# Kernel optimization log

Measured on AMD Instinct MI355X. Metric: run time of the kernel, lower is better.

The kernel has to match this reference:

```python
import jax, jax.numpy as jnp
import numpy as np

B, S, V, I, H = 32, 512, 8000, 256, 512
LN_EPS = 1e-5


def setup_inputs() -> dict:
    key = jax.random.key(0)
    ks = jax.random.split(key, 8)
    norm = lambda k, shp, sc: jax.random.normal(k, shp, dtype=jnp.float32) * sc
    return {
        "x_idx": jax.random.randint(ks[0], (B, S), 0, V),
        "emb": norm(ks[1], (V, I), 1.0),                    # nn.Embedding weight
        "W_in": norm(ks[2], (H, I), 1.0 / np.sqrt(I)),       # input_proj
        "b_in": jnp.zeros((H,), jnp.float32),
        "W_rec": norm(ks[3], (H, H), 1.0 / np.sqrt(H)),      # recurrent_proj
        "b_rec": jnp.zeros((H,), jnp.float32),
        "W_tr": norm(ks[4], (H, H), 1.0 / np.sqrt(H)),       # trunk linear
        "b_tr": jnp.zeros((H,), jnp.float32),
        "gamma": jnp.ones((H,), jnp.float32),                # shared LayerNorm
        "beta": jnp.zeros((H,), jnp.float32),
        "W_out": norm(ks[5], (V, H), 1.0 / np.sqrt(H)),      # output_proj
        "b_out": jnp.zeros((V,), jnp.float32),
    }


def reference(x_idx, emb, W_in, b_in, W_rec, b_rec, W_tr, b_tr, gamma, beta, W_out, b_out):
    bsz = x_idx.shape[0]

    def layer_norm(x):
        m = jnp.mean(x, axis=-1, keepdims=True)
        v = jnp.mean((x - m) ** 2, axis=-1, keepdims=True)
        return (x - m) * jax.lax.rsqrt(v + LN_EPS) * gamma + beta

    xs = emb[x_idx]                     # [B,S,I] gather all embeddings up front
    xs_t = jnp.swapaxes(xs, 0, 1)       # [S,B,I] for scan over time

    def step(h, x_t):
        h_t = jnp.tanh(x_t @ W_in.T + b_in + h @ W_rec.T + b_rec)   # [B,H]
        h_new = layer_norm(jnp.tanh(h_t @ W_tr.T + b_tr))           # trunk (layer_count=1)
        return h_new, h_new

    h0 = jnp.zeros((bsz, W_in.shape[0]), xs.dtype)
    _, hs = jax.lax.scan(step, h0, xs_t)                            # hs: [S,B,H]

    # output projection is out of the recurrence -> batch it after the scan
    y_s = jnp.einsum('sbh,vh->bsv', hs, W_out) + b_out              # [B,S,V]
    return y_s
```

## Files before the change

### kernel.cpp

```cpp
#include <hip/hip_runtime.h>
#include <hip/hip_bf16.h>

#define B_ 32
#define S_ 512
#define V_ 8000
#define I_ 256
#define H_ 512
#define LN_EPS 1e-5f
#define NSL 16
#define NBP 8
#define NBLK 128
#define PHALF (NBP * NSL * 4 * 512)

#define OFF_WR   0
#define OFF_WT   16512
#define OFF_HB   33024
#define OFF_HTS  35088
#define OFF_RED  35220
#define OFF_RED2 37268
#define LDSF     37284

static __device__ __forceinline__ unsigned short f2bf(float x) {
    __hip_bfloat16 h = __float2bfloat16(x);
    return *reinterpret_cast<unsigned short*>(&h);
}

__global__ void k_transpose(const float* __restrict__ in, float* __restrict__ out,
                            int R, int C) {
    __shared__ float tile[32][33];
    int c0 = blockIdx.x * 32, r0 = blockIdx.y * 32;
    int tx = threadIdx.x, ty = threadIdx.y;
#pragma unroll
    for (int i = 0; i < 32; i += 8)
        tile[ty + i][tx] = in[(size_t)(r0 + ty + i) * C + (c0 + tx)];
    __syncthreads();
#pragma unroll
    for (int i = 0; i < 32; i += 8)
        out[(size_t)(c0 + ty + i) * R + (r0 + tx)] = tile[tx][ty + i];
}

__global__ __launch_bounds__(256) void k_cvt_bf16(const float* __restrict__ in,
                                                  unsigned short* __restrict__ out, int n4) {
    for (int i = blockIdx.x * 256 + threadIdx.x; i < n4; i += gridDim.x * 256) {
        float4 v = ((const float4*)in)[i];
        ushort4 o;
        o.x = f2bf(v.x); o.y = f2bf(v.y); o.z = f2bf(v.z); o.w = f2bf(v.w);
        ((ushort4*)out)[i] = o;
    }
}

__global__ __launch_bounds__(512) void k_embed_proj(
        const int* __restrict__ x_idx, const float* __restrict__ emb,
        const float* __restrict__ WinT, const float* __restrict__ b_in,
        float* __restrict__ Xp) {
    __shared__ float e[8][I_];
    const int m0 = blockIdx.x * 8;
    const int t = threadIdx.x;
    {
        int r = t >> 6, i4 = (t & 63) * 4;
        int m = m0 + r;
        int s = m >> 5, b = m & 31;
        int idx = x_idx[b * S_ + s];
        *(float4*)&e[r][i4] = *(const float4*)&emb[(size_t)idx * I_ + i4];
    }
    __syncthreads();
    const int j = t;
    float acc[8];
    const float bj = b_in[j];
#pragma unroll
    for (int r = 0; r < 8; ++r) acc[r] = bj;
    for (int i = 0; i < I_; ++i) {
        float w = WinT[(size_t)i * H_ + j];
#pragma unroll
        for (int r = 0; r < 8; ++r) acc[r] += e[r][i] * w;
    }
#pragma unroll
    for (int r = 0; r < 8; ++r)
        Xp[(size_t)(m0 + r) * H_ + j] = acc[r];
}

__global__ __launch_bounds__(512) void k_scan_1b(
        const float* __restrict__ Xp,
        const float* __restrict__ W_rec, const float* __restrict__ b_rec,
        const float* __restrict__ W_tr,  const float* __restrict__ b_tr,
        const float* __restrict__ gamma, const float* __restrict__ beta,
        float* __restrict__ pP, unsigned int* __restrict__ flags,
        unsigned short* __restrict__ hsB) {
    extern __shared__ float sm[];
    float*  WrS  = sm + OFF_WR;
    float*  WtS  = sm + OFF_WT;
    float*  hb   = sm + OFF_HB;
    float*  hts  = sm + OFF_HTS;
    float*  red  = sm + OFF_RED;
    float2* red2 = (float2*)(sm + OFF_RED2);

    const int bid = blockIdx.x;
    const int bp = bid >> 4, g = bid & 15;
    const int t = threadIdx.x;
    const int j = t & 31, kc = t >> 5;
    const int rB = t >> 7, jB = (t & 127) << 2;
    const int wid = t >> 6;

    for (int idx = t; idx < 32 * 512; idx += 512) {
        int jj = idx >> 9, k = idx & 511;
        WrS[jj * 516 + k] = W_rec[(size_t)(g * 32 + jj) * H_ + k];
    }
    for (int idx = t; idx < 512 * 32; idx += 512) {
        int jj = idx >> 5, kl = idx & 31;
        WtS[kl * 516 + jj] = W_tr[(size_t)jj * H_ + g * 32 + kl];
    }
    const float brj = b_rec[g * 32 + j];
    const float4 bt4 = *(const float4*)&b_tr[jB];
    const float4 gm4 = *(const float4*)&gamma[jB];
    const float4 be4 = *(const float4*)&beta[jB];
    __syncthreads();

    for (int s = 0; s < S_; ++s) {
        float xv = 0.f;
        if (t < 128) xv = Xp[((size_t)s * B_ + bp * 4 + (t >> 5)) * H_ + g * 32 + (t & 31)];

        {
            float a0 = 0, a1 = 0, a2 = 0, a3 = 0;
            if (s > 0) {
                const int kbase = kc * 32;
#pragma unroll
                for (int i = 0; i < 8; ++i) {
                    const int k4 = kbase + i * 4;
                    const float4 w4 = *(const float4*)&WrS[j * 516 + k4];
                    const float4 h0 = *(const float4*)&hb[0 * 516 + k4];
                    const float4 h1 = *(const float4*)&hb[1 * 516 + k4];
                    const float4 h2 = *(const float4*)&hb[2 * 516 + k4];
                    const float4 h3 = *(const float4*)&hb[3 * 516 + k4];
                    a0 += h0.x * w4.x + h0.y * w4.y + h0.z * w4.z + h0.w * w4.w;
                    a1 += h1.x * w4.x + h1.y * w4.y + h1.z * w4.z + h1.w * w4.w;
                    a2 += h2.x * w4.x + h2.y * w4.y + h2.z * w4.z + h2.w * w4.w;
                    a3 += h3.x * w4.x + h3.y * w4.y + h3.z * w4.z + h3.w * w4.w;
                }
            }
            red[kc * 128 + 0 * 32 + j] = a0;
            red[kc * 128 + 1 * 32 + j] = a1;
            red[kc * 128 + 2 * 32 + j] = a2;
            red[kc * 128 + 3 * 32 + j] = a3;
        }
        __syncthreads();
        if (t < 128) {
            const int r2 = t >> 5, j2 = t & 31;
            float sum = 0.f;
#pragma unroll
            for (int c = 0; c < 16; ++c) sum += red[c * 128 + r2 * 32 + j2];
            hts[r2 * 33 + j2] = tanhf(sum + xv + brj);
        }
        __syncthreads();

        {
            float4 pa = {0.f, 0.f, 0.f, 0.f};
            const float* hrow = hts + rB * 33;
#pragma unroll 8
            for (int kl = 0; kl < 32; ++kl) {
                const float hv = hrow[kl];
                const float4 w4 = *(const float4*)&WtS[kl * 516 + jB];
                pa.x += hv * w4.x; pa.y += hv * w4.y;
                pa.z += hv * w4.z; pa.w += hv * w4.w;
            }
            const size_t pb = (size_t)(s & 1) * PHALF
                            + (size_t)(bp * 16 + g) * 2048 + rB * 512 + jB;
            union { float2 f; unsigned long long u; } q0, q1;
            q0.f = make_float2(pa.x, pa.y);
            q1.f = make_float2(pa.z, pa.w);
            __hip_atomic_store((unsigned long long*)&pP[pb], q0.u,
                               __ATOMIC_RELAXED, __HIP_MEMORY_SCOPE_AGENT);
            __hip_atomic_store((unsigned long long*)&pP[pb + 2], q1.u,
                               __ATOMIC_RELAXED, __HIP_MEMORY_SCOPE_AGENT);
        }
        __syncthreads();

        if (t == 0)
            __hip_atomic_store(&flags[(bp * 16 + g) * 32], (unsigned)(s + 1),
                               __ATOMIC_RELEASE, __HIP_MEMORY_SCOPE_AGENT);
        if (t < NSL)
            while (__hip_atomic_load(&flags[(bp * 16 + t) * 32],
                       __ATOMIC_RELAXED, __HIP_MEMORY_SCOPE_AGENT) < (unsigned)(s + 1))
                __builtin_amdgcn_s_sleep(1);
        __syncthreads();
        __builtin_amdgcn_sched_barrier(0);

        float u0, u1, u2, u3;
        {
            float a0 = 0, a1 = 0, a2 = 0, a3 = 0;
            const unsigned long long* gp =
                (const unsigned long long*)(pP + (size_t)(s & 1) * PHALF);
            const int off = rB * 512 + jB;
#pragma unroll
            for (int gg = 0; gg < 16; ++gg) {
                const size_t base = ((size_t)(bp * 16 + gg) * 2048 + off) >> 1;
                unsigned long long v0 = __hip_atomic_load(&gp[base],
                                           __ATOMIC_RELAXED, __HIP_MEMORY_SCOPE_AGENT);
                unsigned long long v1 = __hip_atomic_load(&gp[base + 1],
                                           __ATOMIC_RELAXED, __HIP_MEMORY_SCOPE_AGENT);
                union { unsigned long long u; float2 f; } w0, w1;
                w0.u = v0; w1.u = v1;
                a0 += w0.f.x; a1 += w0.f.y; a2 += w1.f.x; a3 += w1.f.y;
            }
            u0 = tanhf(a0 + bt4.x); u1 = tanhf(a1 + bt4.y);
            u2 = tanhf(a2 + bt4.z); u3 = tanhf(a3 + bt4.w);
            float s1 = (u0 + u1) + (u2 + u3);
            float s2 = (u0 * u0 + u1 * u1) + (u2 * u2 + u3 * u3);
#pragma unroll
            for (int o = 1; o < 64; o <<= 1) {
                s1 += __shfl_xor(s1, o);
                s2 += __shfl_xor(s2, o);
            }
            if ((t & 63) == 0) red2[wid] = make_float2(s1, s2);
        }
        __syncthreads();

        {
            const float2 A = red2[rB * 2], Bv = red2[rB * 2 + 1];
            const float mean = (A.x + Bv.x) * (1.0f / H_);
            const float var  = (A.y + Bv.y) * (1.0f / H_) - mean * mean;
            const float rs = rsqrtf(var + LN_EPS);
            float4 hn;
            hn.x = (u0 - mean) * rs * gm4.x + be4.x;
            hn.y = (u1 - mean) * rs * gm4.y + be4.y;
            hn.z = (u2 - mean) * rs * gm4.z + be4.z;
            hn.w = (u3 - mean) * rs * gm4.w + be4.w;
            *(float4*)&hb[rB * 516 + jB] = hn;
            if ((jB >> 5) == g) {
                ushort4 o;
                o.x = f2bf(hn.x); o.y = f2bf(hn.y);
                o.z = f2bf(hn.z); o.w = f2bf(hn.w);
                *(ushort4*)&hsB[((size_t)s * B_ + bp * 4 + rB) * H_ + jB] = o;
            }
        }
        __syncthreads();
    }
}

typedef __attribute__((ext_vector_type(8))) short short8;
typedef __attribute__((ext_vector_type(4))) float f32x4;

__global__ __launch_bounds__(256) void k_out_mfma(
        const unsigned short* __restrict__ hsB, const unsigned short* __restrict__ WoB,
        const float* __restrict__ b_out, float* __restrict__ y) {
    __shared__ unsigned short As[128 * 40];
    __shared__ unsigned short Bs[128 * 40];

    const int v0 = blockIdx.x * 128;
    const int m0 = blockIdx.y * 128;
    const int t = threadIdx.x;
    const int l = t & 63, wv = t >> 6;
    const int wm = wv >> 1, wn = wv & 1;

    f32x4 acc[4][4];
#pragma unroll
    for (int i = 0; i < 4; ++i)
#pragma unroll
        for (int jq = 0; jq < 4; ++jq)
            acc[i][jq] = (f32x4){0.f, 0.f, 0.f, 0.f};

    float bias[4];
#pragma unroll
    for (int ni = 0; ni < 4; ++ni) {
        int v = v0 + wn * 64 + ni * 16 + (l & 15);
        bias[ni] = (v < V_) ? b_out[v] : 0.f;
    }

    for (int k0 = 0; k0 < H_; k0 += 32) {
        __syncthreads();
        for (int c = t; c < 512; c += 256) {
            int row = c >> 2, seg = c & 3;
            *(uint4*)&As[row * 40 + seg * 8] =
                *(const uint4*)&hsB[(size_t)(m0 + row) * H_ + k0 + seg * 8];
            int vr = v0 + row; if (vr > V_ - 1) vr = V_ - 1;
            *(uint4*)&Bs[row * 40 + seg * 8] =
                *(const uint4*)&WoB[(size_t)vr * H_ + k0 + seg * 8];
        }
        __syncthreads();

        short8 af[4], bf[4];
#pragma unroll
        for (int i = 0; i < 4; ++i) {
            af[i] = *(short8*)&As[(wm * 64 + i * 16 + (l & 15)) * 40 + (l >> 4) * 8];
            bf[i] = *(short8*)&Bs[(wn * 64 + i * 16 + (l & 15)) * 40 + (l >> 4) * 8];
        }
#pragma unroll
        for (int mi = 0; mi < 4; ++mi)
#pragma unroll
            for (int ni = 0; ni < 4; ++ni)
                acc[mi][ni] = __builtin_amdgcn_mfma_f32_16x16x32_bf16(
                    af[mi], bf[ni], acc[mi][ni], 0, 0, 0);
    }

#pragma unroll
    for (int mi = 0; mi < 4; ++mi) {
#pragma unroll
        for (int ni = 0; ni < 4; ++ni) {
            int vcol = v0 + wn * 64 + ni * 16 + (l & 15);
            if (vcol < V_) {
#pragma unroll
                for (int p = 0; p < 4; ++p) {
                    int m = m0 + wm * 64 + mi * 16 + (l >> 4) * 4 + p;
                    int s = m >> 5, b = m & 31;
                    y[((size_t)b * S_ + s) * V_ + vcol] = acc[mi][ni][p] + bias[ni];
                }
            }
        }
    }
}

extern "C" void kernel_launch(void* const* d_in, const int* in_sizes, int n_in,
                              void* d_out, int out_size, void* d_ws, size_t ws_size,
                              hipStream_t stream) {
    const int*   x_idx = (const int*)d_in[0];
    const float* emb   = (const float*)d_in[1];
    const float* W_in  = (const float*)d_in[2];
    const float* b_in  = (const float*)d_in[3];
    const float* W_rec = (const float*)d_in[4];
    const float* b_rec = (const float*)d_in[5];
    const float* W_tr  = (const float*)d_in[6];
    const float* b_tr  = (const float*)d_in[7];
    const float* gamma = (const float*)d_in[8];
    const float* beta  = (const float*)d_in[9];
    const float* W_out = (const float*)d_in[10];
    const float* b_out = (const float*)d_in[11];
    float* y  = (float*)d_out;
    float* ws = (float*)d_ws;

    float* WinT = ws;
    float* Xp   = ws + 131072;
    unsigned short* hsB = (unsigned short*)(ws + 8519680);
    unsigned short* WoB = (unsigned short*)(ws + 12713984);
    float* pP   = ws + 14761984;
    unsigned int* flags = (unsigned int*)(ws + 15286272);

    (void)hipFuncSetAttribute((const void*)k_scan_1b,
                              hipFuncAttributeMaxDynamicSharedMemorySize,
                              LDSF * 4);

    dim3 tb(32, 8);
    k_transpose<<<dim3(I_ / 32, H_ / 32), tb, 0, stream>>>(W_in, WinT, H_, I_);

    k_cvt_bf16<<<1024, 256, 0, stream>>>(W_out, WoB, V_ * H_ / 4);

    k_embed_proj<<<(B_ * S_) / 8, 512, 0, stream>>>(x_idx, emb, WinT, b_in, Xp);

    hipMemsetAsync(flags, 0, NBLK * 32 * sizeof(unsigned int), stream);

    k_scan_1b<<<NBLK, 512, LDSF * 4, stream>>>(Xp, W_rec, b_rec, W_tr, b_tr,
                                               gamma, beta, pP, flags, hsB);

    k_out_mfma<<<dim3((V_ + 127) / 128, (B_ * S_) / 128), 256, 0, stream>>>(
        hsB, WoB, b_out, y);
}
```

Baseline: 4.449 ms.

## Replace flag barrier with sentinel-polled triple-buffered partial sums in scan

```diff
diff --git a/kernel.cpp b/kernel.cpp
--- a/kernel.cpp
+++ b/kernel.cpp
@@ -10,7 +10,8 @@
 #define NSL 16
 #define NBP 8
 #define NBLK 128
-#define PHALF (NBP * NSL * 4 * 512)
+#define PHALF (NBLK * 2048)
+#define SENT 0xFFFFFFFFFFFFFFFFull
 
 #define OFF_WR   0
 #define OFF_WT   16512
@@ -79,13 +80,12 @@
         Xp[(size_t)(m0 + r) * H_ + j] = acc[r];
 }
 
-__global__ __launch_bounds__(512) void k_scan_1b(
+__global__ __launch_bounds__(512, 2) void k_scan_poll(
         const float* __restrict__ Xp,
         const float* __restrict__ W_rec, const float* __restrict__ b_rec,
         const float* __restrict__ W_tr,  const float* __restrict__ b_tr,
         const float* __restrict__ gamma, const float* __restrict__ beta,
-        float* __restrict__ pP, unsigned int* __restrict__ flags,
-        unsigned short* __restrict__ hsB) {
+        float* __restrict__ pP, unsigned short* __restrict__ hsB) {
     extern __shared__ float sm[];
     float*  WrS  = sm + OFF_WR;
     float*  WtS  = sm + OFF_WT;
@@ -100,6 +100,7 @@
     const int j = t & 31, kc = t >> 5;
     const int rB = t >> 7, jB = (t & 127) << 2;
     const int wid = t >> 6;
+    const size_t roff64 = (size_t)(rB * 512 + jB) >> 1;
 
     for (int idx = t; idx < 32 * 512; idx += 512) {
         int jj = idx >> 9, k = idx & 511;
@@ -152,8 +153,8 @@
         }
         __syncthreads();
 
-        {
-            float4 pa = {0.f, 0.f, 0.f, 0.f};
+        float4 pa = {0.f, 0.f, 0.f, 0.f};
+        {
             const float* hrow = hts + rB * 33;
 #pragma unroll 8
             for (int kl = 0; kl < 32; ++kl) {
@@ -162,43 +163,57 @@
                 pa.x += hv * w4.x; pa.y += hv * w4.y;
                 pa.z += hv * w4.z; pa.w += hv * w4.w;
             }
-            const size_t pb = (size_t)(s & 1) * PHALF
-                            + (size_t)(bp * 16 + g) * 2048 + rB * 512 + jB;
-            union { float2 f; unsigned long long u; } q0, q1;
-            q0.f = make_float2(pa.x, pa.y);
-            q1.f = make_float2(pa.z, pa.w);
-            __hip_atomic_store((unsigned long long*)&pP[pb], q0.u,
-                               __ATOMIC_RELAXED, __HIP_MEMORY_SCOPE_AGENT);
-            __hip_atomic_store((unsigned long long*)&pP[pb + 2], q1.u,
-                               __ATOMIC_RELAXED, __HIP_MEMORY_SCOPE_AGENT);
-        }
-        __syncthreads();
-
-        if (t == 0)
-            __hip_atomic_store(&flags[(bp * 16 + g) * 32], (unsigned)(s + 1),
-                               __ATOMIC_RELEASE, __HIP_MEMORY_SCOPE_AGENT);
-        if (t < NSL)
-            while (__hip_atomic_load(&flags[(bp * 16 + t) * 32],
-                       __ATOMIC_RELAXED, __HIP_MEMORY_SCOPE_AGENT) < (unsigned)(s + 1))
+        }
+        union { float2 f; unsigned long long u; } q0, q1;
+        q0.f = make_float2(pa.x, pa.y);
+        q1.f = make_float2(pa.z, pa.w);
+        unsigned long long* pw =
+            (unsigned long long*)(pP + (size_t)(s % 3) * PHALF);
+        {
+            const size_t myb = (size_t)(bp * 16 + g) * 1024 + roff64;
+            __hip_atomic_store(&pw[myb], q0.u, __ATOMIC_RELAXED, __HIP_MEMORY_SCOPE_AGENT);
+            __hip_atomic_store(&pw[myb + 1], q1.u, __ATOMIC_RELAXED, __HIP_MEMORY_SCOPE_AGENT);
+        }
+
+        unsigned long long va[16], vb[16];
+        va[g] = q0.u; vb[g] = q1.u;
+#pragma unroll
+        for (int gg = 0; gg < 16; ++gg) {
+            if (gg != g) {
+                const size_t base = (size_t)(bp * 16 + gg) * 1024 + roff64;
+                va[gg] = __hip_atomic_load(&pw[base], __ATOMIC_RELAXED, __HIP_MEMORY_SCOPE_AGENT);
+                vb[gg] = __hip_atomic_load(&pw[base + 1], __ATOMIC_RELAXED, __HIP_MEMORY_SCOPE_AGENT);
+            }
+        }
+        {
+            unsigned got = 1u << g;
+            while (1) {
+#pragma unroll
+                for (int gg = 0; gg < 16; ++gg) {
+                    if (!(got & (1u << gg)) && va[gg] != SENT && vb[gg] != SENT)
+                        got |= 1u << gg;
+                }
+                if (got == 0xFFFFu) break;
                 __builtin_amdgcn_s_sleep(1);
-        __syncthreads();
-        __builtin_amdgcn_sched_barrier(0);
-
+#pragma unroll
+                for (int gg = 0; gg < 16; ++gg) {
+                    if (!(got & (1u << gg))) {
+                        const size_t base = (size_t)(bp * 16 + gg) * 1024 + roff64;
+                        if (va[gg] == SENT)
+                            va[gg] = __hip_atomic_load(&pw[base], __ATOMIC_RELAXED, __HIP_MEMORY_SCOPE_AGENT);
+                        if (vb[gg] == SENT)
+                            vb[gg] = __hip_atomic_load(&pw[base + 1], __ATOMIC_RELAXED, __HIP_MEMORY_SCOPE_AGENT);
+                    }
+                }
+            }
+        }
         float u0, u1, u2, u3;
         {
             float a0 = 0, a1 = 0, a2 = 0, a3 = 0;
-            const unsigned long long* gp =
-                (const unsigned long long*)(pP + (size_t)(s & 1) * PHALF);
-            const int off = rB * 512 + jB;
 #pragma unroll
             for (int gg = 0; gg < 16; ++gg) {
-                const size_t base = ((size_t)(bp * 16 + gg) * 2048 + off) >> 1;
-                unsigned long long v0 = __hip_atomic_load(&gp[base],
-                                           __ATOMIC_RELAXED, __HIP_MEMORY_SCOPE_AGENT);
-                unsigned long long v1 = __hip_atomic_load(&gp[base + 1],
-                                           __ATOMIC_RELAXED, __HIP_MEMORY_SCOPE_AGENT);
                 union { unsigned long long u; float2 f; } w0, w1;
-                w0.u = v0; w1.u = v1;
+                w0.u = va[gg]; w1.u = vb[gg];
                 a0 += w0.f.x; a1 += w0.f.y; a2 += w1.f.x; a3 += w1.f.y;
             }
             u0 = tanhf(a0 + bt4.x); u1 = tanhf(a1 + bt4.y);
@@ -211,6 +226,14 @@
                 s2 += __shfl_xor(s2, o);
             }
             if ((t & 63) == 0) red2[wid] = make_float2(s1, s2);
+        }
+
+        {
+            unsigned long long* sw =
+                (unsigned long long*)(pP + (size_t)((s + 2) % 3) * PHALF);
+            const size_t myb = (size_t)(bp * 16 + g) * 1024 + roff64;
+            __hip_atomic_store(&sw[myb], SENT, __ATOMIC_RELAXED, __HIP_MEMORY_SCOPE_AGENT);
+            __hip_atomic_store(&sw[myb + 1], SENT, __ATOMIC_RELAXED, __HIP_MEMORY_SCOPE_AGENT);
         }
         __syncthreads();
 
@@ -331,9 +354,8 @@
     unsigned short* hsB = (unsigned short*)(ws + 8519680);
     unsigned short* WoB = (unsigned short*)(ws + 12713984);
     float* pP   = ws + 14761984;
-    unsigned int* flags = (unsigned int*)(ws + 15286272);
-
-    (void)hipFuncSetAttribute((const void*)k_scan_1b,
+
+    (void)hipFuncSetAttribute((const void*)k_scan_poll,
                               hipFuncAttributeMaxDynamicSharedMemorySize,
                               LDSF * 4);
 
@@ -344,10 +366,10 @@
 
     k_embed_proj<<<(B_ * S_) / 8, 512, 0, stream>>>(x_idx, emb, WinT, b_in, Xp);
 
-    hipMemsetAsync(flags, 0, NBLK * 32 * sizeof(unsigned int), stream);
-
-    k_scan_1b<<<NBLK, 512, LDSF * 4, stream>>>(Xp, W_rec, b_rec, W_tr, b_tr,
-                                               gamma, beta, pP, flags, hsB);
+    hipMemsetAsync(pP, 0xFF, 3 * (size_t)PHALF * sizeof(float), stream);
+
+    k_scan_poll<<<NBLK, 512, LDSF * 4, stream>>>(Xp, W_rec, b_rec, W_tr, b_tr,
+                                                 gamma, beta, pP, hsB);
 
     k_out_mfma<<<dim3((V_ + 127) / 128, (B_ * S_) / 128), 256, 0, stream>>>(
         hsB, WoB, b_out, y);
```

Result: slower. 9.729 ms (+118.7%).

## Co-locate scan block groups on one XCD and use L2-coherent vector exchange

Applied to the files above, without the earlier changes.

```diff
diff --git a/kernel.cpp b/kernel.cpp
--- a/kernel.cpp
+++ b/kernel.cpp
@@ -10,7 +10,7 @@
 #define NSL 16
 #define NBP 8
 #define NBLK 128
-#define PHALF (NBP * NSL * 4 * 512)
+#define PHALF (NBLK * 2048)
 
 #define OFF_WR   0
 #define OFF_WT   16512
@@ -18,7 +18,11 @@
 #define OFF_HTS  35088
 #define OFF_RED  35220
 #define OFF_RED2 37268
-#define LDSF     37284
+#define OFF_MISC 37284
+#define LDSF     37288
+
+typedef __attribute__((ext_vector_type(4))) float f32x4;
+typedef __attribute__((ext_vector_type(8))) short short8;
 
 static __device__ __forceinline__ unsigned short f2bf(float x) {
     __hip_bfloat16 h = __float2bfloat16(x);
@@ -79,13 +83,13 @@
         Xp[(size_t)(m0 + r) * H_ + j] = acc[r];
 }
 
-__global__ __launch_bounds__(512) void k_scan_1b(
+__global__ __launch_bounds__(512, 2) void k_scan_xcd2(
         const float* __restrict__ Xp,
         const float* __restrict__ W_rec, const float* __restrict__ b_rec,
         const float* __restrict__ W_tr,  const float* __restrict__ b_tr,
         const float* __restrict__ gamma, const float* __restrict__ beta,
         float* __restrict__ pP, unsigned int* __restrict__ flags,
-        unsigned short* __restrict__ hsB) {
+        unsigned int* __restrict__ xccs, unsigned short* __restrict__ hsB) {
     extern __shared__ float sm[];
     float*  WrS  = sm + OFF_WR;
     float*  WtS  = sm + OFF_WT;
@@ -95,7 +99,7 @@
     float2* red2 = (float2*)(sm + OFF_RED2);
 
     const int bid = blockIdx.x;
-    const int bp = bid >> 4, g = bid & 15;
+    const int g = bid >> 3, bp = bid & 7;
     const int t = threadIdx.x;
     const int j = t & 31, kc = t >> 5;
     const int rB = t >> 7, jB = (t & 127) << 2;
@@ -113,7 +117,29 @@
     const float4 bt4 = *(const float4*)&b_tr[jB];
     const float4 gm4 = *(const float4*)&gamma[jB];
     const float4 be4 = *(const float4*)&beta[jB];
+
+    unsigned xcc;
+    asm volatile("s_getreg_b32 %0, hwreg(HW_REG_XCC_ID)" : "=s"(xcc));
+    xcc &= 0xffu;
+    if (t == 0)
+        __hip_atomic_store(&xccs[bid], xcc, __ATOMIC_RELAXED, __HIP_MEMORY_SCOPE_AGENT);
+    {
+        int ok = 1;
+        if (t < NSL) {
+            unsigned v;
+            do {
+                v = __hip_atomic_load(&xccs[t * 8 + bp],
+                                      __ATOMIC_RELAXED, __HIP_MEMORY_SCOPE_AGENT);
+                if (v == 0xFFFFFFFFu) __builtin_amdgcn_s_sleep(1);
+            } while (v == 0xFFFFFFFFu);
+            ok = (v == xcc) ? 1 : 0;
+        }
+        unsigned long long bal = __ballot(ok);
+        if (t == 0)
+            ((int*)sm)[OFF_MISC] = (bal == ~0ull) ? 1 : 0;
+    }
     __syncthreads();
+    const bool fast = ((int*)sm)[OFF_MISC] != 0;
 
     for (int s = 0; s < S_; ++s) {
         float xv = 0.f;
@@ -152,8 +178,8 @@
         }
         __syncthreads();
 
-        {
-            float4 pa = {0.f, 0.f, 0.f, 0.f};
+        float4 pa = {0.f, 0.f, 0.f, 0.f};
+        {
             const float* hrow = hts + rB * 33;
 #pragma unroll 8
             for (int kl = 0; kl < 32; ++kl) {
@@ -162,44 +188,69 @@
                 pa.x += hv * w4.x; pa.y += hv * w4.y;
                 pa.z += hv * w4.z; pa.w += hv * w4.w;
             }
-            const size_t pb = (size_t)(s & 1) * PHALF
-                            + (size_t)(bp * 16 + g) * 2048 + rB * 512 + jB;
-            union { float2 f; unsigned long long u; } q0, q1;
-            q0.f = make_float2(pa.x, pa.y);
-            q1.f = make_float2(pa.z, pa.w);
-            __hip_atomic_store((unsigned long long*)&pP[pb], q0.u,
-                               __ATOMIC_RELAXED, __HIP_MEMORY_SCOPE_AGENT);
-            __hip_atomic_store((unsigned long long*)&pP[pb + 2], q1.u,
-                               __ATOMIC_RELAXED, __HIP_MEMORY_SCOPE_AGENT);
-        }
+        }
+        {
+            float* pdst = pP + (size_t)(s & 1) * PHALF
+                        + (size_t)bp * 32768 + g * 2048 + (rB * 512 + jB);
+            if (fast) {
+                f32x4 pv = {pa.x, pa.y, pa.z, pa.w};
+                asm volatile("global_store_dwordx4 %0, %1, off sc0"
+                             :: "v"(pdst), "v"(pv) : "memory");
+            } else {
+                union { float2 f; unsigned long long u; } q0, q1;
+                q0.f = make_float2(pa.x, pa.y);
+                q1.f = make_float2(pa.z, pa.w);
+                __hip_atomic_store((unsigned long long*)pdst, q0.u,
+                                   __ATOMIC_RELAXED, __HIP_MEMORY_SCOPE_AGENT);
+                __hip_atomic_store((unsigned long long*)pdst + 1, q1.u,
+                                   __ATOMIC_RELAXED, __HIP_MEMORY_SCOPE_AGENT);
+            }
+        }
+        asm volatile("s_waitcnt vmcnt(0)" ::: "memory");
         __syncthreads();
 
         if (t == 0)
-            __hip_atomic_store(&flags[(bp * 16 + g) * 32], (unsigned)(s + 1),
+            __hip_atomic_store(&flags[(bp * 16 + g) * 16], (unsigned)(s + 1),
                                __ATOMIC_RELEASE, __HIP_MEMORY_SCOPE_AGENT);
         if (t < NSL)
-            while (__hip_atomic_load(&flags[(bp * 16 + t) * 32],
+            while (__hip_atomic_load(&flags[(bp * 16 + t) * 16],
                        __ATOMIC_RELAXED, __HIP_MEMORY_SCOPE_AGENT) < (unsigned)(s + 1))
                 __builtin_amdgcn_s_sleep(1);
         __syncthreads();
         __builtin_amdgcn_sched_barrier(0);
 
+        f32x4 vv[16];
+        {
+            const float* gbase = pP + (size_t)(s & 1) * PHALF
+                               + (size_t)bp * 32768 + (rB * 512 + jB);
+            if (fast) {
+#pragma unroll
+                for (int gg = 0; gg < 16; ++gg)
+                    asm volatile("global_load_dwordx4 %0, %1, off sc0"
+                                 : "=v"(vv[gg]) : "v"(gbase + gg * 2048) : "memory");
+                asm volatile("s_waitcnt vmcnt(0)" ::: "memory");
+                __builtin_amdgcn_sched_barrier(0);
+            } else {
+#pragma unroll
+                for (int gg = 0; gg < 16; ++gg) {
+                    const unsigned long long* bp64 =
+                        (const unsigned long long*)(gbase + gg * 2048);
+                    unsigned long long v0 = __hip_atomic_load(bp64,
+                        __ATOMIC_RELAXED, __HIP_MEMORY_SCOPE_AGENT);
+                    unsigned long long v1 = __hip_atomic_load(bp64 + 1,
+                        __ATOMIC_RELAXED, __HIP_MEMORY_SCOPE_AGENT);
+                    union { unsigned long long u; float2 f; } w0, w1;
+                    w0.u = v0; w1.u = v1;
+                    vv[gg] = (f32x4){w0.f.x, w0.f.y, w1.f.x, w1.f.y};
+                }
+            }
+        }
         float u0, u1, u2, u3;
         {
             float a0 = 0, a1 = 0, a2 = 0, a3 = 0;
-            const unsigned long long* gp =
-                (const unsigned long long*)(pP + (size_t)(s & 1) * PHALF);
-            const int off = rB * 512 + jB;
 #pragma unroll
             for (int gg = 0; gg < 16; ++gg) {
-                const size_t base = ((size_t)(bp * 16 + gg) * 2048 + off) >> 1;
-                unsigned long long v0 = __hip_atomic_load(&gp[base],
-                                           __ATOMIC_RELAXED, __HIP_MEMORY_SCOPE_AGENT);
-                unsigned long long v1 = __hip_atomic_load(&gp[base + 1],
-                                           __ATOMIC_RELAXED, __HIP_MEMORY_SCOPE_AGENT);
-                union { unsigned long long u; float2 f; } w0, w1;
-                w0.u = v0; w1.u = v1;
-                a0 += w0.f.x; a1 += w0.f.y; a2 += w1.f.x; a3 += w1.f.y;
+                a0 += vv[gg].x; a1 += vv[gg].y; a2 += vv[gg].z; a3 += vv[gg].w;
             }
             u0 = tanhf(a0 + bt4.x); u1 = tanhf(a1 + bt4.y);
             u2 = tanhf(a2 + bt4.z); u3 = tanhf(a3 + bt4.w);
@@ -235,9 +286,6 @@
         __syncthreads();
     }
 }
-
-typedef __attribute__((ext_vector_type(8))) short short8;
-typedef __attribute__((ext_vector_type(4))) float f32x4;
 
 __global__ __launch_bounds__(256) void k_out_mfma(
         const unsigned short* __restrict__ hsB, const unsigned short* __restrict__ WoB,
@@ -332,8 +380,9 @@
     unsigned short* WoB = (unsigned short*)(ws + 12713984);
     float* pP   = ws + 14761984;
     unsigned int* flags = (unsigned int*)(ws + 15286272);
-
-    (void)hipFuncSetAttribute((const void*)k_scan_1b,
+    unsigned int* xccs  = (unsigned int*)(ws + 15288320);
+
+    (void)hipFuncSetAttribute((const void*)k_scan_xcd2,
                               hipFuncAttributeMaxDynamicSharedMemorySize,
                               LDSF * 4);
 
@@ -344,10 +393,11 @@
 
     k_embed_proj<<<(B_ * S_) / 8, 512, 0, stream>>>(x_idx, emb, WinT, b_in, Xp);
 
-    hipMemsetAsync(flags, 0, NBLK * 32 * sizeof(unsigned int), stream);
-
-    k_scan_1b<<<NBLK, 512, LDSF * 4, stream>>>(Xp, W_rec, b_rec, W_tr, b_tr,
-                                               gamma, beta, pP, flags, hsB);
+    hipMemsetAsync(flags, 0, 2048 * sizeof(unsigned int), stream);
+    hipMemsetAsync(xccs, 0xFF, 128 * sizeof(unsigned int), stream);
+
+    k_scan_xcd2<<<NBLK, 512, LDSF * 4, stream>>>(Xp, W_rec, b_rec, W_tr, b_tr,
+                                                 gamma, beta, pP, flags, xccs, hsB);
 
     k_out_mfma<<<dim3((V_ + 127) / 128, (B_ * S_) / 128), 256, 0, stream>>>(
         hsB, WoB, b_out, y);
```

Result: faster. 3.828 ms (-14.0%).
